# Performance work log

Measured on AMD Instinct MI355X. Metric: run time of the kernel, lower is better.

## Reference

```python
import jax, jax.numpy as jnp
from jax import lax
import numpy as np

B, D, NFM = 4096, 64, 32
N_USER, N_ITEM = 1000000, 100000
DN = ('NCHW', 'OIHW', 'NCHW')


def setup_inputs() -> dict:
    key = jax.random.key(0)
    ks = jax.random.split(key, 10)
    user = jax.random.randint(ks[0], (B, 1), 0, N_USER)
    item_pos = jax.random.randint(ks[1], (B, 1), 0, N_ITEM)
    item_neg = jax.random.randint(ks[2], (B, 1), 0, N_ITEM)
    user_emb_w = jax.random.normal(ks[3], (N_USER, D), dtype=jnp.float32) * 0.1
    item_emb_w = jax.random.normal(ks[4], (N_ITEM, D), dtype=jnp.float32) * 0.1
    # conv1: in_channels=1; convs 2..6: in_channels=NFM (kaiming-ish init)
    conv1_w = jax.random.normal(ks[5], (NFM, 1, 4, 4), dtype=jnp.float32) * 0.35
    conv1_b = jnp.full((NFM,), 0.01, dtype=jnp.float32)
    rest_w = jax.random.normal(ks[6], (5, NFM, NFM, 4, 4), dtype=jnp.float32) * 0.0625
    rest_b = jnp.full((5, NFM), 0.01, dtype=jnp.float32)
    pred_w = jax.random.normal(ks[7], (1, NFM), dtype=jnp.float32) * 0.25
    pred_b = jnp.full((1,), 0.01, dtype=jnp.float32)
    return dict(user=user, item_pos=item_pos, item_neg=item_neg,
                user_emb_w=user_emb_w, item_emb_w=item_emb_w,
                conv1_w=conv1_w, conv1_b=conv1_b, rest_w=rest_w, rest_b=rest_b,
                pred_w=pred_w, pred_b=pred_b)


def _conv(x, w, b):
    y = lax.conv_general_dilated(x, w, window_strides=(2, 2),
                                 padding=[(1, 1), (1, 1)], dimension_numbers=DN)
    return jax.nn.relu(y + b[None, :, None, None])


def _branch(u, it, conv1_w, conv1_b, rest_w, rest_b, pred_w, pred_b):
    # batched outer product replaces the per-sample torch.mm loop: [B,1,64,64]
    x = jnp.einsum('bd,be->bde', u, it)[:, None, :, :]
    x = _conv(x, conv1_w, conv1_b)
    for i in range(rest_w.shape[0]):  # fixed 5 conv layers
        x = _conv(x, rest_w[i], rest_b[i])
    x = x.reshape(x.shape[0], -1)  # [B, NFM] (spatial collapsed to 1x1)
    return jax.nn.sigmoid(x @ pred_w.T + pred_b)


def reference(user, item_pos, item_neg, user_emb_w, item_emb_w,
              conv1_w, conv1_b, rest_w, rest_b, pred_w, pred_b):
    u = user_emb_w[user[:, 0]]          # [B, 64]
    ip = item_emb_w[item_pos[:, 0]]     # [B, 64]
    ineg = item_emb_w[item_neg[:, 0]]   # [B, 64]
    out1 = _branch(u, ip, conv1_w, conv1_b, rest_w, rest_b, pred_w, pred_b)
    out2 = _branch(u, ineg, conv1_w, conv1_b, rest_w, rest_b, pred_w, pred_b)
    return (out1, out2)
```

## Files before the change

### kernel.cpp

```cpp
#include <hip/hip_runtime.h>
#include <math.h>

#define NT 256
#define NW 4

typedef __attribute__((ext_vector_type(8))) short short8;
typedef __attribute__((ext_vector_type(4))) float f32x4;

#define U_OFF    0
#define IT_OFF   256
#define B1_OFF   512
#define RB_OFF   640
#define PW_OFF   1280
#define PBI_OFF  1408
#define ZP_OFF   1424
#define X1_OFF   1536
#define X1_STR   2064
#define T_OFF    36624
#define X2_OFF   55056
#define X2_STR   1040
#define X3_OFF   X1_OFF
#define X3_STR   528
#define X4_OFF   (X1_OFF + 4224)
#define X4_STR   272
#define X5_OFF   (X1_OFF + 5312)
#define X5_STR   144
#define X6_OFF   (X1_OFF + 5600)
#define SMEM_BYTES 71696

__device__ __forceinline__ unsigned short f2bf(float f) {
    unsigned int x = __float_as_uint(f);
    x += 0x7fffu + ((x >> 16) & 1u);
    return (unsigned short)(x >> 16);
}

__device__ __forceinline__ void loadB16(short8 bfr[16], const unsigned short* __restrict__ wsbf,
                                        const float* __restrict__ rwg, int useWs,
                                        int L, int co, int g) {
    if (useWs) {
        const unsigned short* base = wsbf + L * 16384 + co * 32 + g * 8;
#pragma unroll
        for (int tap = 0; tap < 16; ++tap)
            bfr[tap] = *(const short8*)(base + tap * 1024);
    } else {
#pragma unroll
        for (int tap = 0; tap < 16; ++tap) {
            union { short8 s; unsigned short u[8]; } cv;
#pragma unroll
            for (int e = 0; e < 8; ++e)
                cv.u[e] = f2bf(rwg[((L * 32 + co) * 32 + g * 8 + e) * 16 + tap]);
            bfr[tap] = cv.s;
        }
    }
}

template<int PH, int QW, int NIN, int INS, int OUTS, bool LAST>
__device__ __forceinline__ void convL(char* smb, int inOff, int outOff,
                                      const short8 bfr[16], float bias,
                                      int p0, int shift) {
    const int t = threadIdx.x;
    const int w = t >> 6, l = t & 63;
    const int n = l & 15, g = l >> 4, nt = w & 1;
    constexpr int M = PH * QW;
    constexpr int MT = (M + 15) / 16;
    for (int tile = w; tile < 2 * MT; tile += NW) {
        const int mt = tile >> 1;
        f32x4 acc = {bias, bias, bias, bias};
        const int m = mt * 16 + (l & 15);
        const int mm = (m < M) ? m : 0;
        const int p = mm % PH, q = mm / PH;
#pragma unroll
        for (int a = 0; a < 4; ++a)
#pragma unroll
            for (int dj = 0; dj < 4; ++dj) {
                const int row = 2 * (p0 + p) + a - 1;
                const int col = 2 * q + dj - 1;
                const bool ok = (m < M) && ((unsigned)row < (unsigned)NIN)
                                        && ((unsigned)col < (unsigned)NIN);
                const int rb = row - shift;
                unsigned addr = (unsigned)(inOff + rb * INS + col * 64 + g * 16);
                addr ^= (unsigned)(((rb >> 3) & 1) << 4);
                addr = ok ? addr : (unsigned)(ZP_OFF + g * 16);
                short8 af = *(const short8*)(smb + addr);
                acc = __builtin_amdgcn_mfma_f32_16x16x32_bf16(af, bfr[a * 4 + dj], acc, 0, 0, 0);
            }
#pragma unroll
        for (int vi = 0; vi < 4; ++vi) {
            const int mo = mt * 16 + g * 4 + vi;
            if (mo < M) {
                const float v = fmaxf(acc[vi], 0.f);
                if constexpr (LAST) {
                    *(float*)(smb + outOff + (nt * 16 + n) * 4) = v;
                } else {
                    const int po = mo % PH + p0, qo = mo / PH;
                    unsigned addr = (unsigned)(outOff + po * OUTS + qo * 64 + (nt * 16 + n) * 2);
                    addr ^= (unsigned)(((po >> 3) & 1) << 4);
                    *(unsigned short*)(smb + addr) = f2bf(v);
                }
            }
        }
    }
}

__global__ void preconv_w(const float* __restrict__ rwg, unsigned short* __restrict__ wsbf) {
    int idx = blockIdx.x * 256 + threadIdx.x;
    if (idx < 81920) {
        int ci = idx & 31, co = (idx >> 5) & 31, tap = (idx >> 10) & 15, L = idx >> 14;
        wsbf[idx] = f2bf(rwg[(((L * 32 + co) * 32 + ci) << 4) + tap]);
    }
}

__global__ void __launch_bounds__(NT, 2)
convncf_main(const int* __restrict__ user, const int* __restrict__ item_pos,
             const int* __restrict__ item_neg,
             const float* __restrict__ uemb, const float* __restrict__ iemb,
             const float* __restrict__ w1g, const float* __restrict__ b1g,
             const float* __restrict__ rwg, const float* __restrict__ rbg,
             const float* __restrict__ pwg, const float* __restrict__ pbg,
             const unsigned short* __restrict__ wsbf, int useWs,
             float* __restrict__ out, int B)
{
    extern __shared__ char smb[];
    float* smf = (float*)smb;
    const int t = threadIdx.x, w = t >> 6, l = t & 63;
    const int co = ((t >> 6) & 1) * 16 + (t & 15);
    const int g = l >> 4;
    const int s = blockIdx.x, branch = blockIdx.y;
    const int uidx = user[s];
    const int iidx = branch ? item_neg[s] : item_pos[s];

    short8 bfr[16];
    loadB16(bfr, wsbf, rwg, useWs, 0, co, g);

    for (int i = t; i < 353; i += NT) {
        if (i < 64)       smf[U_OFF/4 + i]        = uemb[(long)uidx * 64 + i];
        else if (i < 128) smf[IT_OFF/4 + i - 64]  = iemb[(long)iidx * 64 + i - 64];
        else if (i < 160) smf[B1_OFF/4 + i - 128] = b1g[i - 128];
        else if (i < 320) smf[RB_OFF/4 + i - 160] = rbg[i - 160];
        else if (i < 352) smf[PW_OFF/4 + i - 320] = pwg[i - 320];
        else              smf[PBI_OFF/4] = pbg[0];
    }
    if (t < 4) *(float4*)(smb + ZP_OFF + t * 16) = make_float4(0.f, 0.f, 0.f, 0.f);
    __syncthreads();

    for (int v = t; v < 4096; v += NT) {
        const int ci = v & 31, j = (v >> 5) & 31, a = v >> 10;
        const float4 wv = *(const float4*)(w1g + ci * 16 + a * 4);
        const int c0 = 2 * j - 1;
        const float i0 = (c0 >= 0) ? smf[IT_OFF/4 + c0] : 0.f;
        const float i1 = smf[IT_OFF/4 + c0 + 1];
        const float i2 = smf[IT_OFF/4 + c0 + 2];
        const float i3 = (c0 + 3 < 64) ? smf[IT_OFF/4 + c0 + 3] : 0.f;
        float acc = wv.x * i0;
        acc = fmaf(wv.y, i1, acc);
        acc = fmaf(wv.z, i2, acc);
        acc = fmaf(wv.w, i3, acc);
        *(float*)(smb + T_OFF + (a * 32 + j) * 144 + ci * 4) = acc;
    }
    __syncthreads();

    {
        const int pi = t & 127;
        const int cgp = pi & 3, jp = pi >> 2;
        const int rlh = t >> 7;
        const int rl0 = rlh ? 9 : 0;
        const int rl1 = rlh ? 17 : 9;

        float4 tv[4][2];
#pragma unroll
        for (int a = 0; a < 4; ++a) {
            const float* tp = (const float*)(smb + T_OFF + (a * 32 + jp) * 144 + cgp * 32);
            tv[a][0] = *(const float4*)tp;
            tv[a][1] = *(const float4*)(tp + 4);
        }
        float bb[8];
        {
            const float* b1p = smf + B1_OFF/4 + cgp * 8;
#pragma unroll
            for (int e = 0; e < 8; ++e) bb[e] = b1p[e];
        }

#pragma unroll 1
        for (int h = 0; h < 2; ++h) {
            const int shift = 15 * h;
            for (int rl = rl0; rl < rl1; ++rl) {
                const int r = rl + shift;
                float acc[8];
#pragma unroll
                for (int e = 0; e < 8; ++e) acc[e] = bb[e];
#pragma unroll
                for (int a = 0; a < 4; ++a) {
                    const int m = 2 * r - 1 + a;
                    const float uv = (m >= 0 && m < 64) ? smf[U_OFF/4 + m] : 0.f;
                    acc[0] = fmaf(uv, tv[a][0].x, acc[0]);
                    acc[1] = fmaf(uv, tv[a][0].y, acc[1]);
                    acc[2] = fmaf(uv, tv[a][0].z, acc[2]);
                    acc[3] = fmaf(uv, tv[a][0].w, acc[3]);
                    acc[4] = fmaf(uv, tv[a][1].x, acc[4]);
                    acc[5] = fmaf(uv, tv[a][1].y, acc[5]);
                    acc[6] = fmaf(uv, tv[a][1].z, acc[6]);
                    acc[7] = fmaf(uv, tv[a][1].w, acc[7]);
                }
                union { short8 sv; unsigned short u[8]; } cv;
#pragma unroll
                for (int e = 0; e < 8; ++e) cv.u[e] = f2bf(fmaxf(acc[e], 0.f));
                unsigned addr = (unsigned)(X1_OFF + rl * X1_STR + jp * 64 + cgp * 16);
                addr ^= (unsigned)(((rl >> 3) & 1) << 4);
                *(short8*)(smb + addr) = cv.sv;
            }
            __syncthreads();

            convL<8, 16, 32, X1_STR, X2_STR, false>(smb, X1_OFF, X2_OFF, bfr,
                                                    smf[RB_OFF/4 + co], 8 * h, shift);
            if (h == 1) loadB16(bfr, wsbf, rwg, useWs, 1, co, g);
            __syncthreads();
        }
    }

    convL<8, 8, 16, X2_STR, X3_STR, false>(smb, X2_OFF, X3_OFF, bfr, smf[RB_OFF/4 + 32 + co], 0, 0);
    loadB16(bfr, wsbf, rwg, useWs, 2, co, g);
    __syncthreads();

    convL<4, 4, 8, X3_STR, X4_STR, false>(smb, X3_OFF, X4_OFF, bfr, smf[RB_OFF/4 + 64 + co], 0, 0);
    loadB16(bfr, wsbf, rwg, useWs, 3, co, g);
    __syncthreads();

    convL<2, 2, 4, X4_STR, X5_STR, false>(smb, X4_OFF, X5_OFF, bfr, smf[RB_OFF/4 + 96 + co], 0, 0);
    loadB16(bfr, wsbf, rwg, useWs, 4, co, g);
    __syncthreads();

    convL<1, 1, 2, X5_STR, 0, true>(smb, X5_OFF, X6_OFF, bfr, smf[RB_OFF/4 + 128 + co], 0, 0);
    __syncthreads();

    if (w == 0) {
        float v = (l < 32) ? smf[X6_OFF/4 + l] * smf[PW_OFF/4 + l] : 0.f;
#pragma unroll
        for (int d = 32; d >= 1; d >>= 1) v += __shfl_xor(v, d, 64);
        if (l == 0) {
            const float z = smf[PBI_OFF/4] + v;
            out[branch * B + s] = 1.f / (1.f + expf(-z));
        }
    }
}

extern "C" void kernel_launch(void* const* d_in, const int* in_sizes, int n_in,
                              void* d_out, int out_size, void* d_ws, size_t ws_size,
                              hipStream_t stream) {
    const int*   user     = (const int*)d_in[0];
    const int*   item_pos = (const int*)d_in[1];
    const int*   item_neg = (const int*)d_in[2];
    const float* uemb     = (const float*)d_in[3];
    const float* iemb     = (const float*)d_in[4];
    const float* w1       = (const float*)d_in[5];
    const float* b1       = (const float*)d_in[6];
    const float* rw       = (const float*)d_in[7];
    const float* rb       = (const float*)d_in[8];
    const float* pw       = (const float*)d_in[9];
    const float* pb       = (const float*)d_in[10];
    float* out = (float*)d_out;
    const int B = in_sizes[0];

    const int useWs = (ws_size >= 81920u * sizeof(unsigned short)) ? 1 : 0;
    unsigned short* wsbf = (unsigned short*)d_ws;
    if (useWs)
        preconv_w<<<dim3(320), dim3(256), 0, stream>>>(rw, wsbf);

    (void)hipFuncSetAttribute((const void*)convncf_main,
                              hipFuncAttributeMaxDynamicSharedMemorySize, SMEM_BYTES);
    dim3 grid(B, 2);
    convncf_main<<<grid, NT, SMEM_BYTES, stream>>>(
        user, item_pos, item_neg, uemb, iemb, w1, b1, rw, rb, pw, pb,
        wsbf, useWs, out, B);
}
```

Baseline: 329.4 us.

## Compute conv1 item-side terms in registers and drop shared T buffer

The separate pass that computed conv1 item-weight products into a shared-memory T table, and its barrier, are removed. Each thread now computes its 32 needed values directly in registers from the item embedding and the conv1 weights in global memory. This shrinks shared memory from about 70KB to about 52KB and raises launch bounds to 3 blocks per CU, aiming for higher occupancy and one fewer sync. The cost is redundant per-thread global weight loads and FMAs, and added register pressure under the tighter launch bound.

```diff
diff --git a/kernel.cpp b/kernel.cpp
--- a/kernel.cpp
+++ b/kernel.cpp
@@ -16,8 +16,7 @@
 #define ZP_OFF   1424
 #define X1_OFF   1536
 #define X1_STR   2064
-#define T_OFF    36624
-#define X2_OFF   55056
+#define X2_OFF   36624
 #define X2_STR   1040
 #define X3_OFF   X1_OFF
 #define X3_STR   528
@@ -26,7 +25,7 @@
 #define X5_OFF   (X1_OFF + 5312)
 #define X5_STR   144
 #define X6_OFF   (X1_OFF + 5600)
-#define SMEM_BYTES 71696
+#define SMEM_BYTES 53264
 
 __device__ __forceinline__ unsigned short f2bf(float f) {
     unsigned int x = __float_as_uint(f);
@@ -110,7 +109,7 @@
     }
 }
 
-__global__ void __launch_bounds__(NT, 2)
+__global__ void __launch_bounds__(NT, 3)
 convncf_main(const int* __restrict__ user, const int* __restrict__ item_pos,
              const int* __restrict__ item_neg,
              const float* __restrict__ uemb, const float* __restrict__ iemb,
@@ -143,22 +142,6 @@
     if (t < 4) *(float4*)(smb + ZP_OFF + t * 16) = make_float4(0.f, 0.f, 0.f, 0.f);
     __syncthreads();
 
-    for (int v = t; v < 4096; v += NT) {
-        const int ci = v & 31, j = (v >> 5) & 31, a = v >> 10;
-        const float4 wv = *(const float4*)(w1g + ci * 16 + a * 4);
-        const int c0 = 2 * j - 1;
-        const float i0 = (c0 >= 0) ? smf[IT_OFF/4 + c0] : 0.f;
-        const float i1 = smf[IT_OFF/4 + c0 + 1];
-        const float i2 = smf[IT_OFF/4 + c0 + 2];
-        const float i3 = (c0 + 3 < 64) ? smf[IT_OFF/4 + c0 + 3] : 0.f;
-        float acc = wv.x * i0;
-        acc = fmaf(wv.y, i1, acc);
-        acc = fmaf(wv.z, i2, acc);
-        acc = fmaf(wv.w, i3, acc);
-        *(float*)(smb + T_OFF + (a * 32 + j) * 144 + ci * 4) = acc;
-    }
-    __syncthreads();
-
     {
         const int pi = t & 127;
         const int cgp = pi & 3, jp = pi >> 2;
@@ -166,12 +149,25 @@
         const int rl0 = rlh ? 9 : 0;
         const int rl1 = rlh ? 17 : 9;
 
-        float4 tv[4][2];
-#pragma unroll
-        for (int a = 0; a < 4; ++a) {
-            const float* tp = (const float*)(smb + T_OFF + (a * 32 + jp) * 144 + cgp * 32);
-            tv[a][0] = *(const float4*)tp;
-            tv[a][1] = *(const float4*)(tp + 4);
+        float itv[4];
+#pragma unroll
+        for (int dj = 0; dj < 4; ++dj) {
+            const int c = 2 * jp - 1 + dj;
+            itv[dj] = (c >= 0 && c < 64) ? smf[IT_OFF/4 + c] : 0.f;
+        }
+        float tval[4][8];
+#pragma unroll
+        for (int e = 0; e < 8; ++e) {
+            const float* wp = w1g + (cgp * 8 + e) * 16;
+#pragma unroll
+            for (int a = 0; a < 4; ++a) {
+                const float4 wv = *(const float4*)(wp + a * 4);
+                float v = wv.x * itv[0];
+                v = fmaf(wv.y, itv[1], v);
+                v = fmaf(wv.z, itv[2], v);
+                v = fmaf(wv.w, itv[3], v);
+                tval[a][e] = v;
+            }
         }
         float bb[8];
         {
@@ -192,14 +188,9 @@
                 for (int a = 0; a < 4; ++a) {
                     const int m = 2 * r - 1 + a;
                     const float uv = (m >= 0 && m < 64) ? smf[U_OFF/4 + m] : 0.f;
-                    acc[0] = fmaf(uv, tv[a][0].x, acc[0]);
-                    acc[1] = fmaf(uv, tv[a][0].y, acc[1]);
-                    acc[2] = fmaf(uv, tv[a][0].z, acc[2]);
-                    acc[3] = fmaf(uv, tv[a][0].w, acc[3]);
-                    acc[4] = fmaf(uv, tv[a][1].x, acc[4]);
-                    acc[5] = fmaf(uv, tv[a][1].y, acc[5]);
-                    acc[6] = fmaf(uv, tv[a][1].z, acc[6]);
-                    acc[7] = fmaf(uv, tv[a][1].w, acc[7]);
+#pragma unroll
+                    for (int e = 0; e < 8; ++e)
+                        acc[e] = fmaf(uv, tval[a][e], acc[e]);
                 }
                 union { short8 sv; unsigned short u[8]; } cv;
 #pragma unroll
```

Result: slower. 400.3 us (+21.6%).
